# Kernel optimization log

Measured on AMD Instinct MI355X. Metric: run time of the kernel, lower is better.

## Reference

```python
import jax, jax.numpy as jnp
import numpy as np

R, B, D = 1024, 16, 1024
K_ACTIVE = 20
FB_DECAY = 0.9          # feedback_decay
REFR_W = 1.0            # refractory_weight
FB_W = 0.5              # feedback_weight


def _hex_neighbors(rows=32, cols=32):
    """Toroidal hex grid adjacency: 6 neighbors per region, shape [R, 6]."""
    n = rows * cols
    idx = np.arange(n)
    r, c = idx // cols, idx % cols
    def wrap(rr, cc):
        return (rr % rows) * cols + (cc % cols)
    nbrs = np.stack([
        wrap(r, c - 1), wrap(r, c + 1),
        wrap(r - 1, c), wrap(r + 1, c),
        wrap(r - 1, c + 1), wrap(r + 1, c - 1),
    ], axis=1)
    return nbrs.astype(np.int32)


def setup_inputs() -> dict:
    key = jax.random.key(0)
    k1, k2, k3, k4, k5 = jax.random.split(key, 5)
    return {
        "H": jax.random.normal(k1, (R, B, D), jnp.float32),
        "neighbor_msg": jax.random.normal(k2, (R, B, D), jnp.float32),
        "w": jax.random.normal(k3, (D,), jnp.float32) / np.float32(np.sqrt(D)),
        "theta": jnp.zeros((R,), jnp.float32),
        "refractory": jax.random.uniform(k4, (B, R), jnp.float32),
        "feedback": jax.random.uniform(k5, (B, R), jnp.float32),
        "neighbor_indices": jnp.asarray(_hex_neighbors()),
    }


def _greedy_hex_nms(adj, nbrs, k):
    """adj: [B, R] adjusted scores; nbrs: [R, 6]. Returns hard mask [B, R]."""
    n_regions = adj.shape[1]

    def nms_one(scores):
        order = jnp.argsort(-scores)  # descending

        def step(state, idx):
            sel, sup, cnt = state
            take = (cnt < k) & (~sel[idx]) & (~sup[idx])
            sel = sel.at[idx].set(sel[idx] | take)
            sup = sup.at[idx].set(sup[idx] | take)
            nb = nbrs[idx]  # [6]
            sup = sup.at[nb].set(sup[nb] | take)
            return (sel, sup, cnt + take.astype(jnp.int32)), None

        init = (jnp.zeros(n_regions, bool), jnp.zeros(n_regions, bool), jnp.int32(0))
        (sel, _, _), _ = jax.lax.scan(step, init, order)
        return sel.astype(scores.dtype)

    return jax.vmap(nms_one)(adj)


def reference(H, neighbor_msg, w, theta, refractory, feedback, neighbor_indices):
    # learned score: Linear(D, 1, bias=False) -> [B, R]
    s = jnp.einsum('rbd,d->br', H, w)
    # feedback inhibition from routed message magnitude
    fb_mag = jnp.linalg.norm(neighbor_msg, axis=-1).T          # [B, R]
    fb_new = FB_DECAY * feedback + (1.0 - FB_DECAY) * fb_mag   # updated _feedback
    adj = s - theta[None, :] - REFR_W * refractory - FB_W * fb_new
    hard = jax.lax.stop_gradient(_greedy_hex_nms(adj, neighbor_indices, K_ACTIVE))
    soft = jax.nn.sigmoid(adj)
    ste = hard + soft - jax.lax.stop_gradient(soft)            # straight-through
    Hs = H * ste.T[:, :, None]                                 # [R, B, D]
    return Hs, hard, adj
```

## Files before the change

kernel.cpp:

```cpp
#include <hip/hip_runtime.h>
#include <hip/hip_bf16.h>
#include <math.h>

#define RR 1024
#define BB 16
#define DD 1024
#define K_ACTIVE 20

__global__ __launch_bounds__(256) void score_kernel(
    const float* __restrict__ H, const float* __restrict__ msg,
    const float* __restrict__ w, const float* __restrict__ theta,
    const float* __restrict__ refr, const float* __restrict__ fb,
    float* __restrict__ adj_out)
{
    const int wave = threadIdx.x >> 6;
    const int lane = threadIdx.x & 63;
    const int pair = blockIdx.x * 4 + wave;
    const int r = pair >> 4;
    const int b = pair & 15;

    const float4* H4 = (const float4*)(H + (size_t)pair * DD);
    const float4* M4 = (const float4*)(msg + (size_t)pair * DD);
    const float4* W4 = (const float4*)w;

    float dot = 0.f, ss = 0.f;
#pragma unroll
    for (int k = 0; k < 4; ++k) {
        const int i = lane + 64 * k;
        const float4 h = H4[i];
        const float4 m = M4[i];
        const float4 ww = W4[i];
        dot += h.x * ww.x + h.y * ww.y + h.z * ww.z + h.w * ww.w;
        ss  += m.x * m.x + m.y * m.y + m.z * m.z + m.w * m.w;
    }
#pragma unroll
    for (int off = 32; off > 0; off >>= 1) {
        dot += __shfl_down(dot, off);
        ss  += __shfl_down(ss, off);
    }
    if (lane == 0) {
        const float fb_mag = sqrtf(ss);
        const float fb_new = 0.9f * fb[b * RR + r] + 0.1f * fb_mag;
        const float a = dot - theta[r] - refr[b * RR + r] - 0.5f * fb_new;
        adj_out[b * RR + r] = a;
    }
}

__global__ __launch_bounds__(256) void nms_kernel(
    const float* __restrict__ adj, const int* __restrict__ nbrs,
    float* __restrict__ hard)
{
    __shared__ float val[RR];
    __shared__ unsigned char sel[RR];
    __shared__ float wv[4];
    __shared__ int wi[4];

    const int b = blockIdx.x;
    const int tid = threadIdx.x;
    const int lane = tid & 63;
    const int wave = tid >> 6;

#pragma unroll
    for (int j = 0; j < 4; ++j) {
        const int i = tid + 256 * j;
        val[i] = adj[b * RR + i];
        sel[i] = 0;
    }
    __syncthreads();

    for (int it = 0; it < K_ACTIVE; ++it) {
        float m = -INFINITY;
        int mi = RR;
#pragma unroll
        for (int j = 0; j < 4; ++j) {
            const int i = tid + 256 * j;
            const float v = val[i];
            if (v > m || (v == m && i < mi)) { m = v; mi = i; }
        }
#pragma unroll
        for (int off = 32; off > 0; off >>= 1) {
            const float ov = __shfl_down(m, off);
            const int   oi = __shfl_down(mi, off);
            if (ov > m || (ov == m && oi < mi)) { m = ov; mi = oi; }
        }
        if (lane == 0) { wv[wave] = m; wi[wave] = mi; }
        __syncthreads();
        if (tid == 0) {
            float bm = wv[0];
            int bi = wi[0];
#pragma unroll
            for (int q = 1; q < 4; ++q) {
                if (wv[q] > bm || (wv[q] == bm && wi[q] < bi)) { bm = wv[q]; bi = wi[q]; }
            }
            if (bm > -INFINITY) {
                sel[bi] = 1;
                val[bi] = -INFINITY;
#pragma unroll
                for (int j = 0; j < 6; ++j) val[nbrs[bi * 6 + j]] = -INFINITY;
            }
        }
        __syncthreads();
    }

#pragma unroll
    for (int j = 0; j < 4; ++j) {
        const int i = tid + 256 * j;
        hard[b * RR + i] = sel[i] ? 1.0f : 0.0f;
    }
}

__global__ __launch_bounds__(256) void gate_kernel(
    const float* __restrict__ H, const float* __restrict__ hard,
    float* __restrict__ Hs)
{
    const int pair = blockIdx.x;
    const int r = pair >> 4;
    const int b = pair & 15;
    const float g = hard[b * RR + r];

    float4* out4 = (float4*)(Hs + (size_t)pair * DD);
    if (g != 0.0f) {
        const float4* H4 = (const float4*)(H + (size_t)pair * DD);
        out4[threadIdx.x] = H4[threadIdx.x];
    } else {
        out4[threadIdx.x] = make_float4(0.f, 0.f, 0.f, 0.f);
    }
}

extern "C" void kernel_launch(void* const* d_in, const int* in_sizes, int n_in,
                              void* d_out, int out_size, void* d_ws, size_t ws_size,
                              hipStream_t stream) {
    const float* H     = (const float*)d_in[0];
    const float* msg   = (const float*)d_in[1];
    const float* w     = (const float*)d_in[2];
    const float* theta = (const float*)d_in[3];
    const float* refr  = (const float*)d_in[4];
    const float* fb    = (const float*)d_in[5];
    const int*   nbrs  = (const int*)d_in[6];

    float* out  = (float*)d_out;
    float* Hs   = out;
    float* hard = out + (size_t)RR * BB * DD;
    float* adj  = hard + (size_t)BB * RR;

    score_kernel<<<RR * BB / 4, 256, 0, stream>>>(H, msg, w, theta, refr, fb, adj);
    nms_kernel<<<BB, 256, 0, stream>>>(adj, nbrs, hard);
    gate_kernel<<<RR * BB, 256, 0, stream>>>(H, hard, Hs);
}
```

Measured before the change: 209.8 us.

## Use single-wave NMS, wave-per-row gating with nontemporal stores, hoisted score loads

The score kernel now issues all twelve vector loads up front before doing any arithmetic, which exposes more memory-level parallelism. NMS runs as a single 64-lane wave that caches the neighbor table in shared memory and picks the argmax with a shuffle broadcast, removing the cross-wave reduction and one barrier per iteration. The gate kernel assigns one wave per (r,b) row and four rows per block, and writes with nontemporal stores to cut launch granularity and cache pollution on the large output. The risk is that the single-wave NMS scans 16 elements per lane serially, and the nontemporal stores may behave differently from plain stores on this cache hierarchy.

New measurement: 209.9 us. About the same (+0.0%).

```diff
diff --git a/kernel.cpp b/kernel.cpp
--- a/kernel.cpp
+++ b/kernel.cpp
@@ -6,6 +6,8 @@
 #define BB 16
 #define DD 1024
 #define K_ACTIVE 20
+
+typedef float vfloat4 __attribute__((ext_vector_type(4)));
 
 __global__ __launch_bounds__(256) void score_kernel(
     const float* __restrict__ H, const float* __restrict__ msg,
@@ -19,20 +21,27 @@
     const int r = pair >> 4;
     const int b = pair & 15;
 
-    const float4* H4 = (const float4*)(H + (size_t)pair * DD);
-    const float4* M4 = (const float4*)(msg + (size_t)pair * DD);
-    const float4* W4 = (const float4*)w;
+    const vfloat4* __restrict__ H4 = (const vfloat4*)(H + (size_t)pair * DD);
+    const vfloat4* __restrict__ M4 = (const vfloat4*)(msg + (size_t)pair * DD);
+    const vfloat4* __restrict__ W4 = (const vfloat4*)w;
 
-    float dot = 0.f, ss = 0.f;
-#pragma unroll
-    for (int k = 0; k < 4; ++k) {
-        const int i = lane + 64 * k;
-        const float4 h = H4[i];
-        const float4 m = M4[i];
-        const float4 ww = W4[i];
-        dot += h.x * ww.x + h.y * ww.y + h.z * ww.z + h.w * ww.w;
-        ss  += m.x * m.x + m.y * m.y + m.z * m.z + m.w * m.w;
-    }
+    const vfloat4 h0 = H4[lane],       h1 = H4[lane + 64];
+    const vfloat4 h2 = H4[lane + 128], h3 = H4[lane + 192];
+    const vfloat4 m0 = M4[lane],       m1 = M4[lane + 64];
+    const vfloat4 m2 = M4[lane + 128], m3 = M4[lane + 192];
+    const vfloat4 w0 = W4[lane],       w1 = W4[lane + 64];
+    const vfloat4 w2 = W4[lane + 128], w3 = W4[lane + 192];
+
+    float dot = h0.x * w0.x + h0.y * w0.y + h0.z * w0.z + h0.w * w0.w;
+    dot += h1.x * w1.x + h1.y * w1.y + h1.z * w1.z + h1.w * w1.w;
+    dot += h2.x * w2.x + h2.y * w2.y + h2.z * w2.z + h2.w * w2.w;
+    dot += h3.x * w3.x + h3.y * w3.y + h3.z * w3.z + h3.w * w3.w;
+
+    float ss = m0.x * m0.x + m0.y * m0.y + m0.z * m0.z + m0.w * m0.w;
+    ss += m1.x * m1.x + m1.y * m1.y + m1.z * m1.z + m1.w * m1.w;
+    ss += m2.x * m2.x + m2.y * m2.y + m2.z * m2.z + m2.w * m2.w;
+    ss += m3.x * m3.x + m3.y * m3.y + m3.z * m3.z + m3.w * m3.w;
+
 #pragma unroll
     for (int off = 32; off > 0; off >>= 1) {
         dot += __shfl_down(dot, off);
@@ -41,39 +50,40 @@
     if (lane == 0) {
         const float fb_mag = sqrtf(ss);
         const float fb_new = 0.9f * fb[b * RR + r] + 0.1f * fb_mag;
-        const float a = dot - theta[r] - refr[b * RR + r] - 0.5f * fb_new;
-        adj_out[b * RR + r] = a;
+        adj_out[b * RR + r] = dot - theta[r] - refr[b * RR + r] - 0.5f * fb_new;
     }
 }
 
-__global__ __launch_bounds__(256) void nms_kernel(
+__global__ __launch_bounds__(64) void nms_kernel(
     const float* __restrict__ adj, const int* __restrict__ nbrs,
     float* __restrict__ hard)
 {
     __shared__ float val[RR];
+    __shared__ int   nb[RR * 6];
     __shared__ unsigned char sel[RR];
-    __shared__ float wv[4];
-    __shared__ int wi[4];
 
     const int b = blockIdx.x;
-    const int tid = threadIdx.x;
-    const int lane = tid & 63;
-    const int wave = tid >> 6;
+    const int lane = threadIdx.x;
 
 #pragma unroll
-    for (int j = 0; j < 4; ++j) {
-        const int i = tid + 256 * j;
+    for (int j = 0; j < 16; ++j) {
+        const int i = lane + 64 * j;
         val[i] = adj[b * RR + i];
         sel[i] = 0;
     }
+    const int4* nb4g = (const int4*)nbrs;
+    int4* nb4s = (int4*)nb;
+#pragma unroll
+    for (int j = 0; j < 24; ++j)
+        nb4s[lane + 64 * j] = nb4g[lane + 64 * j];
     __syncthreads();
 
     for (int it = 0; it < K_ACTIVE; ++it) {
         float m = -INFINITY;
         int mi = RR;
 #pragma unroll
-        for (int j = 0; j < 4; ++j) {
-            const int i = tid + 256 * j;
+        for (int j = 0; j < 16; ++j) {
+            const int i = lane + 64 * j;
             const float v = val[i];
             if (v > m || (v == m && i < mi)) { m = v; mi = i; }
         }
@@ -83,28 +93,18 @@
             const int   oi = __shfl_down(mi, off);
             if (ov > m || (ov == m && oi < mi)) { m = ov; mi = oi; }
         }
-        if (lane == 0) { wv[wave] = m; wi[wave] = mi; }
-        __syncthreads();
-        if (tid == 0) {
-            float bm = wv[0];
-            int bi = wi[0];
-#pragma unroll
-            for (int q = 1; q < 4; ++q) {
-                if (wv[q] > bm || (wv[q] == bm && wi[q] < bi)) { bm = wv[q]; bi = wi[q]; }
-            }
-            if (bm > -INFINITY) {
-                sel[bi] = 1;
-                val[bi] = -INFINITY;
-#pragma unroll
-                for (int j = 0; j < 6; ++j) val[nbrs[bi * 6 + j]] = -INFINITY;
-            }
+        const int   bi = __shfl(mi, 0);
+        const float bm = __shfl(m, 0);
+        if (bm > -INFINITY) {
+            if (lane == 0) { sel[bi] = 1; val[bi] = -INFINITY; }
+            if (lane < 6)  { val[nb[bi * 6 + lane]] = -INFINITY; }
         }
         __syncthreads();
     }
 
 #pragma unroll
-    for (int j = 0; j < 4; ++j) {
-        const int i = tid + 256 * j;
+    for (int j = 0; j < 16; ++j) {
+        const int i = lane + 64 * j;
         hard[b * RR + i] = sel[i] ? 1.0f : 0.0f;
     }
 }
@@ -113,17 +113,28 @@
     const float* __restrict__ H, const float* __restrict__ hard,
     float* __restrict__ Hs)
 {
-    const int pair = blockIdx.x;
+    const int wave = threadIdx.x >> 6;
+    const int lane = threadIdx.x & 63;
+    const int pair = blockIdx.x * 4 + wave;
     const int r = pair >> 4;
     const int b = pair & 15;
     const float g = hard[b * RR + r];
 
-    float4* out4 = (float4*)(Hs + (size_t)pair * DD);
+    vfloat4* out4 = (vfloat4*)(Hs + (size_t)pair * DD);
     if (g != 0.0f) {
-        const float4* H4 = (const float4*)(H + (size_t)pair * DD);
-        out4[threadIdx.x] = H4[threadIdx.x];
+        const vfloat4* H4 = (const vfloat4*)(H + (size_t)pair * DD);
+        const vfloat4 v0 = H4[lane],       v1 = H4[lane + 64];
+        const vfloat4 v2 = H4[lane + 128], v3 = H4[lane + 192];
+        __builtin_nontemporal_store(v0, &out4[lane]);
+        __builtin_nontemporal_store(v1, &out4[lane + 64]);
+        __builtin_nontemporal_store(v2, &out4[lane + 128]);
+        __builtin_nontemporal_store(v3, &out4[lane + 192]);
     } else {
-        out4[threadIdx.x] = make_float4(0.f, 0.f, 0.f, 0.f);
+        const vfloat4 z = {0.f, 0.f, 0.f, 0.f};
+        __builtin_nontemporal_store(z, &out4[lane]);
+        __builtin_nontemporal_store(z, &out4[lane + 64]);
+        __builtin_nontemporal_store(z, &out4[lane + 128]);
+        __builtin_nontemporal_store(z, &out4[lane + 192]);
     }
 }
 
@@ -144,6 +155,6 @@
     float* adj  = hard + (size_t)BB * RR;
 
     score_kernel<<<RR * BB / 4, 256, 0, stream>>>(H, msg, w, theta, refr, fb, adj);
-    nms_kernel<<<BB, 256, 0, stream>>>(adj, nbrs, hard);
-    gate_kernel<<<RR * BB, 256, 0, stream>>>(H, hard, Hs);
+    nms_kernel<<<BB, 64, 0, stream>>>(adj, nbrs, hard);
+    gate_kernel<<<RR * BB / 4, 256, 0, stream>>>(H, hard, Hs);
 }
```
